# Optimization experiments

Hardware: AMD Instinct MI355X
Metric: run time of the kernel (lower is better)

The kernel has to match this reference:

```python
import jax, jax.numpy as jnp
import numpy as np

NUM_POS_FEATS = 16
TEMPERATURE = 10000.0
SCALE = 100.0

def sine_pos_embed(x):
    # x: [..., 1] -> [..., NUM_POS_FEATS], interleaved sin/cos per torch get_sine_pos_embed
    i = jnp.arange(NUM_POS_FEATS, dtype=jnp.float32)
    dim_t = TEMPERATURE ** (2.0 * jnp.floor(i / 2.0) / NUM_POS_FEATS)
    emb = x * SCALE / dim_t  # [..., NUM_POS_FEATS]
    s = jnp.sin(emb[..., 0::2])
    c = jnp.cos(emb[..., 1::2])
    return jnp.stack([s, c], axis=-1).reshape(emb.shape)

def setup_inputs() -> dict:
    key = jax.random.key(0)
    ks = jax.random.split(key, 6)
    B, N, D, V, H = 4, 900, 256, 16, 8
    queries = jax.random.normal(ks[0], (B, N, D), jnp.float32)
    current_ref_points = jax.random.uniform(ks[1], (B, N, 4), dtype=jnp.float32)
    prev_ref_points = jax.random.uniform(ks[2], (B, N, 4), dtype=jnp.float32)
    vote_w = jax.random.normal(ks[3], (V * 2, D), jnp.float32) * (1.0 / np.sqrt(D))
    vote_b = jnp.zeros((V * 2,), jnp.float32)
    proj_w = jax.random.normal(ks[4], (H, NUM_POS_FEATS), jnp.float32) * 0.25
    proj_b = jnp.zeros((H,), jnp.float32)
    return {"queries": queries, "current_ref_points": current_ref_points,
            "prev_ref_points": prev_ref_points, "vote_w": vote_w, "vote_b": vote_b,
            "proj_w": proj_w, "proj_b": proj_b}

def reference(queries, current_ref_points, prev_ref_points, vote_w, vote_b, proj_w, proj_b):
    B, N, D = queries.shape
    V = vote_w.shape[0] // 2
    # vote_generator: MLP with num_layers=1 == single Linear
    votes = (queries @ vote_w.T + vote_b).reshape(B, N, V, 2)
    vote_pos = current_ref_points[:, :, None, :2] + votes  # [B,N,V,2]
    centers = current_ref_points[:, :, :2]                  # [B,N,2]
    vf = vote_pos.reshape(B, N * V, 2)
    # squared euclidean distances [B, N*V, N] (cdist then **2)
    d2 = (jnp.sum(vf ** 2, -1)[:, :, None]
          + jnp.sum(centers ** 2, -1)[:, None, :]
          - 2.0 * jnp.einsum('bik,bjk->bij', vf, centers))
    d2 = jnp.maximum(d2, 0.0)
    sigma = jnp.mean(current_ref_points[:, :, 2:], -1, keepdims=True) / 2.0  # [B,N,1]
    sigma_flat = jnp.tile(sigma, (1, V, 1))  # faithful to torch .repeat(1,V,1)
    scores = jnp.exp(-d2 / (2.0 * sigma_flat ** 2))          # [B,N*V,N]
    imap = scores.reshape(B, N, V, N).sum(2)                  # vote-sum -> [B,N,N]
    imap = imap / jnp.maximum(jnp.sum(jnp.abs(imap), 2, keepdims=True), 1e-12)  # F.normalize p=1
    imap = 1.0 - imap
    pos = sine_pos_embed(imap[..., None])                     # [B,N,N,16]
    # pos_proj: 1x1 conv (bias) + ReLU over channel dim
    out = jnp.einsum('bnmf,hf->bhnm', pos, proj_w) + proj_b[None, :, None, None]
    return jax.nn.relu(out)
```

## Files before the change

kernel.cpp:

```cpp
#include <hip/hip_runtime.h>

#define NPF 16
#define NH 8
#define NV 16
#define NN 900
#define ND 256
#define NB 4
#define NM (NN * NN)
#define TOTAL (NB * NM)
#define EPB 1024

__global__ __launch_bounds__(256) void hough_imap(
    const float* __restrict__ queries,
    const float* __restrict__ cur_ref,
    const float* __restrict__ vote_w,
    const float* __restrict__ vote_b,
    float* __restrict__ xbuf)
{
    __shared__ __align__(16) float qs[ND];
    __shared__ float part[256];
    __shared__ float vp[NV * 2];
    __shared__ float s2i[NV];
    __shared__ __align__(16) float4 sCoef[NV];
    __shared__ float red[4];
    __shared__ float s_inv;

    const int tid = threadIdx.x;
    const int bn  = blockIdx.x;
    const int b   = bn / NN;
    const int n   = bn - b * NN;

    qs[tid] = queries[(size_t)bn * ND + tid];
    __syncthreads();

    {
        const int o     = tid & 31;
        const int chunk = tid >> 5;
        const float4* wv = (const float4*)(vote_w + o * ND + chunk * 32);
        const float4* qv = (const float4*)(qs + chunk * 32);
        float p = 0.f;
#pragma unroll
        for (int j = 0; j < 8; j++) {
            float4 w4 = wv[j];
            float4 q4 = qv[j];
            p += w4.x * q4.x + w4.y * q4.y + w4.z * q4.z + w4.w * q4.w;
        }
        part[tid] = p;
    }
    __syncthreads();

    if (tid < 32) {
        float s = vote_b[tid];
#pragma unroll
        for (int c = 0; c < 8; c++) s += part[c * 32 + tid];
        vp[tid] = s + cur_ref[((size_t)b * NN + n) * 4 + (tid & 1)];
    } else if (tid >= 64 && tid < 64 + NV) {
        int v = tid - 64;
        int j = (n * NV + v) % NN;
        float c2 = cur_ref[((size_t)b * NN + j) * 4 + 2];
        float c3 = cur_ref[((size_t)b * NN + j) * 4 + 3];
        float sg = (c2 + c3) * 0.25f;
        s2i[v] = 0.5f / (sg * sg);
    }
    __syncthreads();

    if (tid < NV) {
        float x  = vp[2 * tid];
        float y  = vp[2 * tid + 1];
        float s2 = s2i[tid];
        sCoef[tid] = make_float4(2.f * s2 * x, 2.f * s2 * y,
                                 -s2 * (x * x + y * y), -s2);
    }
    __syncthreads();

    float acc[4] = {0.f, 0.f, 0.f, 0.f};
    const float4* cr4 = (const float4*)cur_ref + (size_t)b * NN;

#pragma unroll 1
    for (int c = 0; c < 2; c++) {
        float ax[8], ay[8], c0[8], ns[8];
#pragma unroll
        for (int v = 0; v < 8; v++) {
            float4 f = sCoef[c * 8 + v];
            ax[v] = f.x; ay[v] = f.y; c0[v] = f.z; ns[v] = f.w;
        }
#pragma unroll
        for (int i = 0; i < 4; i++) {
            int m = tid + 256 * i;
            if (m < NN) {
                float4 cr = cr4[m];
                float cx = cr.x, cy = cr.y;
                float cc = cx * cx + cy * cy;
                float a = 0.f;
#pragma unroll
                for (int v = 0; v < 8; v++) {
                    float t = fmaf(ax[v], cx, c0[v]);
                    t = fmaf(ay[v], cy, t);
                    t = fmaf(ns[v], cc, t);
                    a += __expf(fminf(t, 0.f));
                }
                acc[i] += a;
            }
        }
    }

    float lsum = acc[0] + acc[1] + acc[2] + acc[3];
#pragma unroll
    for (int off = 32; off > 0; off >>= 1) lsum += __shfl_down(lsum, off, 64);
    if ((tid & 63) == 0) red[tid >> 6] = lsum;
    __syncthreads();
    if (tid == 0)
        s_inv = 1.0f / fmaxf(red[0] + red[1] + red[2] + red[3], 1e-12f);
    __syncthreads();
    const float inv = s_inv;

    float* xr = xbuf + (size_t)bn * NN;
#pragma unroll
    for (int i = 0; i < 4; i++) {
        int m = tid + 256 * i;
        if (m < NN) xr[m] = 1.0f - acc[i] * inv;
    }
}

__device__ __forceinline__ float uload(const float* p) {
    return __int_as_float(__builtin_amdgcn_readfirstlane(__float_as_int(*p)));
}

__global__ __launch_bounds__(256)
__attribute__((amdgpu_waves_per_eu(4, 4)))
void hough_epi(
    const float* __restrict__ xbuf,
    const float* __restrict__ proj_w,
    const float* __restrict__ proj_b,
    float* __restrict__ out)
{
    const int tid  = threadIdx.x;
    const int base = blockIdx.x * EPB + tid;

    const float invt[8] = {100.0f, 31.622776601683793f, 10.0f, 3.1622776601683795f,
                           1.0f, 0.31622776601683794f, 0.1f, 0.031622776601683791f};

    float sk[4][8], ck[4][8];
    float* op[4];
    bool ok[4];
#pragma unroll
    for (int i = 0; i < 4; i++) {
        int id = base + 256 * i;
        ok[i] = (id < TOTAL);
        float x = ok[i] ? xbuf[id] : 0.f;
#pragma unroll
        for (int k = 0; k < 8; k++) {
            float a = x * invt[k];
            sk[i][k] = __sinf(a);
            ck[i][k] = __cosf(a);
        }
        unsigned int b = (unsigned int)id / (unsigned int)NM;
        unsigned int r = (unsigned int)id - b * (unsigned int)NM;
        op[i] = out + (size_t)b * NH * NM + r;
    }

#pragma unroll 1
    for (int pass = 0; pass < 4; pass++) {
        float w[32];
#pragma unroll
        for (int k = 0; k < 32; k++) w[k] = uload(proj_w + pass * 32 + k);
        const float b0 = uload(proj_b + pass * 2 + 0);
        const float b1 = uload(proj_b + pass * 2 + 1);

#pragma unroll
        for (int i = 0; i < 4; i++) {
            float o0 = b0, o1 = b1;
#pragma unroll
            for (int k = 0; k < 8; k++) {
                o0 = fmaf(w[2 * k],          sk[i][k], o0);
                o0 = fmaf(w[2 * k + 1],      ck[i][k], o0);
                o1 = fmaf(w[16 + 2 * k],     sk[i][k], o1);
                o1 = fmaf(w[16 + 2 * k + 1], ck[i][k], o1);
            }
            if (ok[i]) {
                op[i][(size_t)(pass * 2 + 0) * NM] = fmaxf(o0, 0.f);
                op[i][(size_t)(pass * 2 + 1) * NM] = fmaxf(o1, 0.f);
            }
        }
    }
}

extern "C" void kernel_launch(void* const* d_in, const int* in_sizes, int n_in,
                              void* d_out, int out_size, void* d_ws, size_t ws_size,
                              hipStream_t stream) {
    const float* queries = (const float*)d_in[0];
    const float* cur_ref = (const float*)d_in[1];
    const float* vote_w  = (const float*)d_in[3];
    const float* vote_b  = (const float*)d_in[4];
    const float* proj_w  = (const float*)d_in[5];
    const float* proj_b  = (const float*)d_in[6];
    float* out  = (float*)d_out;
    float* xbuf = (float*)d_ws;

    hough_imap<<<NB * NN, 256, 0, stream>>>(queries, cur_ref, vote_w, vote_b, xbuf);
    hough_epi<<<(TOTAL + EPB - 1) / EPB, 256, 0, stream>>>(xbuf, proj_w, proj_b, out);
}
```

Before: 153.6 us.

## Vectorize epilogue with fp16 dot2 projection and float4 nontemporal stores

Adds a tiny packing kernel that converts the projection weights to packed fp16 pairs. The epilogue now handles four contiguous elements per thread: a float4 load, sin/cos pairs packed to fp16, the 16-wide projection done with fdot2, and float4 nontemporal stores. The aim is to cut VALU work in the projection and make the dominant output writes wider and cache-bypassing. The occupancy hint is raised to match. In exchange it adds an extra launch and lowers the precision of the sin/cos features and weights to fp16 with round-toward-zero.

```diff
diff --git a/kernel.cpp b/kernel.cpp
--- a/kernel.cpp
+++ b/kernel.cpp
@@ -8,7 +8,21 @@
 #define NB 4
 #define NM (NN * NN)
 #define TOTAL (NB * NM)
-#define EPB 1024
+#define TOTAL4 (TOTAL / 4)
+
+typedef __fp16 half2v __attribute__((ext_vector_type(2)));
+typedef float f4v __attribute__((ext_vector_type(4)));
+union h2u { half2v h; unsigned int u; float f; };
+
+#if __has_builtin(__builtin_amdgcn_fdot2)
+__device__ __forceinline__ float fdot2f(half2v a, half2v b, float c) {
+    return __builtin_amdgcn_fdot2(a, b, c, false);
+}
+#else
+__device__ __forceinline__ float fdot2f(half2v a, half2v b, float c) {
+    return fmaf((float)a.x, (float)b.x, fmaf((float)a.y, (float)b.y, c));
+}
+#endif
 
 __global__ __launch_bounds__(256) void hough_imap(
     const float* __restrict__ queries,
@@ -122,66 +136,82 @@
     }
 }
 
-__device__ __forceinline__ float uload(const float* p) {
-    return __int_as_float(__builtin_amdgcn_readfirstlane(__float_as_int(*p)));
+__global__ __launch_bounds__(128) void hough_pack(
+    const float* __restrict__ proj_w,
+    const float* __restrict__ proj_b,
+    unsigned int* __restrict__ wpk)
+{
+    int t = threadIdx.x;
+    if (t < 64) {
+        h2u u;
+        u.h = __builtin_amdgcn_cvt_pkrtz(proj_w[2 * t], proj_w[2 * t + 1]);
+        wpk[t] = u.u;
+    } else if (t < 72) {
+        h2u u;
+        u.f = proj_b[t - 64];
+        wpk[t] = u.u;
+    }
 }
 
 __global__ __launch_bounds__(256)
-__attribute__((amdgpu_waves_per_eu(4, 4)))
+__attribute__((amdgpu_waves_per_eu(6, 8)))
 void hough_epi(
     const float* __restrict__ xbuf,
-    const float* __restrict__ proj_w,
-    const float* __restrict__ proj_b,
+    const unsigned int* __restrict__ wpk,
     float* __restrict__ out)
 {
-    const int tid  = threadIdx.x;
-    const int base = blockIdx.x * EPB + tid;
+    const int t4 = blockIdx.x * 256 + threadIdx.x;
+    if (t4 >= TOTAL4) return;
+
+    const float4 xv = ((const float4*)xbuf)[t4];
+    const float xa[4] = {xv.x, xv.y, xv.z, xv.w};
 
     const float invt[8] = {100.0f, 31.622776601683793f, 10.0f, 3.1622776601683795f,
                            1.0f, 0.31622776601683794f, 0.1f, 0.031622776601683791f};
 
-    float sk[4][8], ck[4][8];
-    float* op[4];
-    bool ok[4];
-#pragma unroll
-    for (int i = 0; i < 4; i++) {
-        int id = base + 256 * i;
-        ok[i] = (id < TOTAL);
-        float x = ok[i] ? xbuf[id] : 0.f;
+    half2v skck[4][8];
+#pragma unroll
+    for (int e = 0; e < 4; e++) {
 #pragma unroll
         for (int k = 0; k < 8; k++) {
-            float a = x * invt[k];
-            sk[i][k] = __sinf(a);
-            ck[i][k] = __cosf(a);
-        }
-        unsigned int b = (unsigned int)id / (unsigned int)NM;
-        unsigned int r = (unsigned int)id - b * (unsigned int)NM;
-        op[i] = out + (size_t)b * NH * NM + r;
-    }
+            float a = xa[e] * invt[k];
+            skck[e][k] = __builtin_amdgcn_cvt_pkrtz(__sinf(a), __cosf(a));
+        }
+    }
+
+    const unsigned int b  = (unsigned int)t4 / 202500u;
+    const unsigned int r4 = (unsigned int)t4 - b * 202500u;
+    float* op = out + (size_t)b * NH * NM + (size_t)r4 * 4;
 
 #pragma unroll 1
     for (int pass = 0; pass < 4; pass++) {
-        float w[32];
-#pragma unroll
-        for (int k = 0; k < 32; k++) w[k] = uload(proj_w + pass * 32 + k);
-        const float b0 = uload(proj_b + pass * 2 + 0);
-        const float b1 = uload(proj_b + pass * 2 + 1);
-
-#pragma unroll
-        for (int i = 0; i < 4; i++) {
-            float o0 = b0, o1 = b1;
+        half2v w0[8], w1[8];
+#pragma unroll
+        for (int k = 0; k < 8; k++) {
+            h2u u0; u0.u = __builtin_amdgcn_readfirstlane(wpk[pass * 16 + k]);
+            h2u u1; u1.u = __builtin_amdgcn_readfirstlane(wpk[pass * 16 + 8 + k]);
+            w0[k] = u0.h; w1[k] = u1.h;
+        }
+        h2u ub0; ub0.u = __builtin_amdgcn_readfirstlane(wpk[64 + 2 * pass]);
+        h2u ub1; ub1.u = __builtin_amdgcn_readfirstlane(wpk[64 + 2 * pass + 1]);
+        const float b0 = ub0.f, b1 = ub1.f;
+
+        float o0[4], o1[4];
+#pragma unroll
+        for (int e = 0; e < 4; e++) {
+            float a0 = b0, a1 = b1;
 #pragma unroll
             for (int k = 0; k < 8; k++) {
-                o0 = fmaf(w[2 * k],          sk[i][k], o0);
-                o0 = fmaf(w[2 * k + 1],      ck[i][k], o0);
-                o1 = fmaf(w[16 + 2 * k],     sk[i][k], o1);
-                o1 = fmaf(w[16 + 2 * k + 1], ck[i][k], o1);
+                a0 = fdot2f(skck[e][k], w0[k], a0);
+                a1 = fdot2f(skck[e][k], w1[k], a1);
             }
-            if (ok[i]) {
-                op[i][(size_t)(pass * 2 + 0) * NM] = fmaxf(o0, 0.f);
-                op[i][(size_t)(pass * 2 + 1) * NM] = fmaxf(o1, 0.f);
-            }
-        }
+            o0[e] = fmaxf(a0, 0.f);
+            o1[e] = fmaxf(a1, 0.f);
+        }
+        f4v s0 = {o0[0], o0[1], o0[2], o0[3]};
+        f4v s1 = {o1[0], o1[1], o1[2], o1[3]};
+        __builtin_nontemporal_store(s0, (f4v*)(op + (size_t)(2 * pass + 0) * NM));
+        __builtin_nontemporal_store(s1, (f4v*)(op + (size_t)(2 * pass + 1) * NM));
     }
 }
 
@@ -196,7 +226,9 @@
     const float* proj_b  = (const float*)d_in[6];
     float* out  = (float*)d_out;
     float* xbuf = (float*)d_ws;
-
+    unsigned int* wpk = (unsigned int*)(xbuf + TOTAL);
+
+    hough_pack<<<1, 128, 0, stream>>>(proj_w, proj_b, wpk);
     hough_imap<<<NB * NN, 256, 0, stream>>>(queries, cur_ref, vote_w, vote_b, xbuf);
-    hough_epi<<<(TOTAL + EPB - 1) / EPB, 256, 0, stream>>>(xbuf, proj_w, proj_b, out);
-}
+    hough_epi<<<(TOTAL4 + 255) / 256, 256, 0, stream>>>(xbuf, wpk, out);
+}
```

Result: slower. 157.4 us (+2.5%).
